# Optimization experiments

Hardware: AMD Instinct MI355X
Metric: run time of the kernel (lower is better)

The kernel has to match this reference:

```python
import jax, jax.numpy as jnp
import numpy as np

N_NODES = 50000
N_EDGES = 400000
IN_FEAT = 988
HIDDEN = 256
CLASSES = 47


def _sage_layer(h, src, dst, W_self, W_neigh, b):
    # DGL SAGEConv 'mean': mean over in-neighbors (messages flow src->dst)
    n = h.shape[0]
    deg = jax.ops.segment_sum(jnp.ones(dst.shape, h.dtype), dst, num_segments=n)
    deg = jnp.maximum(deg, 1.0)  # zero-in-degree nodes -> zero neighbor feature
    agg = jax.ops.segment_sum(h[src], dst, num_segments=n) / deg[:, None]
    return h @ W_self + agg @ W_neigh + b


def setup_inputs() -> dict:
    key = jax.random.key(0)
    ks = jax.random.split(key, 16)
    x = jax.random.normal(ks[0], (N_NODES, IN_FEAT), dtype=jnp.float32)
    src = jax.random.randint(ks[1], (N_EDGES,), 0, N_NODES, dtype=jnp.int32)
    dst = jax.random.randint(ks[2], (N_EDGES,), 0, N_NODES, dtype=jnp.int32)
    dims = [(IN_FEAT, HIDDEN), (HIDDEN, HIDDEN), (HIDDEN, CLASSES)]
    inp = {"x": x, "src": src, "dst": dst}
    for l, (fi, fo) in enumerate(dims):
        s = 1.0 / np.sqrt(fi)
        inp[f"W_self{l}"] = jax.random.normal(ks[3 + 3 * l], (fi, fo), dtype=jnp.float32) * s
        inp[f"W_neigh{l}"] = jax.random.normal(ks[4 + 3 * l], (fi, fo), dtype=jnp.float32) * s
        inp[f"b{l}"] = jnp.zeros((fo,), dtype=jnp.float32)
    return inp


def reference(x, src, dst, W_self0, W_neigh0, b0, W_self1, W_neigh1, b1, W_self2, W_neigh2, b2):
    # feat_size path: h = x, then n_layers SAGEConv layers with relu between
    h = _sage_layer(x, src, dst, W_self0, W_neigh0, b0)
    h = jax.nn.relu(h)
    h = _sage_layer(h, src, dst, W_self1, W_neigh1, b1)
    h = jax.nn.relu(h)
    h = _sage_layer(h, src, dst, W_self2, W_neigh2, b2)
    return h
```

## Files before the change

### kernel.cpp

```cpp
#include <hip/hip_runtime.h>
#include <hip/hip_bf16.h>
#include <cstdint>

#define NODES 50000
#define EDGES 400000
#define FIN   988
#define KP    1024
#define FH    256
#define FC    47

typedef __attribute__((ext_vector_type(8))) short short8;
typedef __attribute__((ext_vector_type(4))) float f32x4;

__device__ __forceinline__ ushort f2bf(float x) {
    union { float f; uint32_t u; } v; v.f = x;
    uint32_t r = v.u + 0x7FFF + ((v.u >> 16) & 1);
    return (ushort)(r >> 16);
}
__device__ __forceinline__ float bf2f(ushort u) {
    union { uint32_t u; float f; } v; v.u = ((uint32_t)u) << 16;
    return v.f;
}
__device__ __forceinline__ void g2l16(const void* g, void* l) {
    __builtin_amdgcn_global_load_lds((const __attribute__((address_space(1))) void*)g,
                                     (__attribute__((address_space(3))) void*)l, 16, 0, 0);
}

__global__ void k_zero(int* __restrict__ p, int n) {
    int i = blockIdx.x * blockDim.x + threadIdx.x;
    if (i < n) p[i] = 0;
}

#define CVTX_BLKS (NODES * (KP / 8) / 256)
#define DEG_BLKS  ((EDGES + 255) / 256)
__global__ void k_cvtx_deg(const float* __restrict__ x, ushort* __restrict__ xbf,
                           const int* __restrict__ dst, int* __restrict__ deg) {
    const int b = blockIdx.x;
    if (b < CVTX_BLKS) {
        int gid = b * 256 + threadIdx.x;
        const int r  = gid >> 7;
        const int kb = (gid & 127) << 3;
        const float* p = x + (size_t)r * FIN + kb;
        short8 o;
        if (kb + 8 <= FIN) {
            f32x4 v0 = *(const f32x4*)(p);
            f32x4 v1 = *(const f32x4*)(p + 4);
#pragma unroll
            for (int i = 0; i < 4; ++i) {
                o[i] = (short)f2bf(v0[i]);
                o[4 + i] = (short)f2bf(v1[i]);
            }
        } else {
#pragma unroll
            for (int i = 0; i < 8; ++i) {
                float f = (kb + i < FIN) ? p[i] : 0.f;
                o[i] = (short)f2bf(f);
            }
        }
        *(short8*)&xbf[(size_t)r * KP + kb] = o;
    } else {
        int i = (b - CVTX_BLKS) * 256 + threadIdx.x;
        if (i < EDGES) atomicAdd(&deg[dst[i]], 1);
    }
}

__global__ __launch_bounds__(256) void k_scan1(const int* __restrict__ deg,
                                               int* __restrict__ bsum, int n) {
    __shared__ int ws[4];
    int i = blockIdx.x * 256 + threadIdx.x;
    int v = (i < n) ? deg[i] : 0;
#pragma unroll
    for (int off = 32; off; off >>= 1) v += __shfl_down(v, off);
    if ((threadIdx.x & 63) == 0) ws[threadIdx.x >> 6] = v;
    __syncthreads();
    if (threadIdx.x == 0) bsum[blockIdx.x] = ws[0] + ws[1] + ws[2] + ws[3];
}

__global__ __launch_bounds__(256) void k_scan2(int* __restrict__ bsum, int nb) {
    __shared__ int s[256];
    int t = threadIdx.x;
    int v = (t < nb) ? bsum[t] : 0;
    s[t] = v;
    __syncthreads();
    for (int off = 1; off < 256; off <<= 1) {
        int u = (t >= off) ? s[t - off] : 0;
        __syncthreads();
        s[t] += u;
        __syncthreads();
    }
    if (t < nb) bsum[t] = s[t] - v;
}

__global__ __launch_bounds__(256) void k_scan3(const int* __restrict__ deg,
                                               const int* __restrict__ bsum,
                                               int* __restrict__ rowptr,
                                               int* __restrict__ cursor, int n) {
    __shared__ int s[256];
    int t = threadIdx.x;
    int i = blockIdx.x * 256 + t;
    int v = (i < n) ? deg[i] : 0;
    s[t] = v;
    __syncthreads();
    for (int off = 1; off < 256; off <<= 1) {
        int u = (t >= off) ? s[t - off] : 0;
        __syncthreads();
        s[t] += u;
        __syncthreads();
    }
    if (i < n) {
        int excl = bsum[blockIdx.x] + s[t] - v;
        rowptr[i] = excl;
        cursor[i] = excl;
    }
    if (i == 0) rowptr[n] = EDGES;
}

#define W0E (512 * KP)
#define W1E (512 * FH)
#define W2E (128 * FH)
#define CVTW_BLKS ((W0E + W1E + W2E + 255) / 256)
__global__ void k_fill_cvtw(const int* __restrict__ src, const int* __restrict__ dst,
                            int* __restrict__ cursor, int* __restrict__ eidx,
                            const float* __restrict__ Ws0, const float* __restrict__ Wn0,
                            const float* __restrict__ Ws1, const float* __restrict__ Wn1,
                            const float* __restrict__ Ws2, const float* __restrict__ Wn2,
                            ushort* __restrict__ Wt0, ushort* __restrict__ Wt1,
                            ushort* __restrict__ Wt2) {
    const int b = blockIdx.x;
    if (b < DEG_BLKS) {
        int i = b * 256 + threadIdx.x;
        if (i < EDGES) {
            int d = dst[i];
            int p = atomicAdd(&cursor[d], 1);
            eidx[p] = src[i];
        }
    } else {
        int gid = (b - DEG_BLKS) * 256 + threadIdx.x;
        if (gid < W0E) {
            int k = gid >> 9, n = gid & 511;
            float v = 0.f;
            if (k < FIN) v = (n < FH) ? Ws0[(size_t)k * FH + n] : Wn0[(size_t)k * FH + (n - FH)];
            Wt0[(size_t)n * KP + k] = f2bf(v);
        } else if (gid < W0E + W1E) {
            int gg = gid - W0E;
            int k = gg >> 9, n = gg & 511;
            float v = (n < FH) ? Ws1[(size_t)k * FH + n] : Wn1[(size_t)k * FH + (n - FH)];
            Wt1[(size_t)n * FH + k] = f2bf(v);
        } else if (gid < W0E + W1E + W2E) {
            int gg = gid - W0E - W1E;
            int k = gg >> 7, n = gg & 127;
            float v = 0.f;
            if (n < FC) v = Ws2[(size_t)k * FC + n];
            else if (n >= 64 && n < 64 + FC) v = Wn2[(size_t)k * FC + (n - 64)];
            Wt2[(size_t)n * FH + k] = f2bf(v);
        }
    }
}

#define TBK 16384

__global__ __launch_bounds__(512, 2) void k_mm256(const ushort* __restrict__ A,
                                                  const ushort* __restrict__ Bt,
                                                  ushort* __restrict__ C,
                                                  const int M, const int lda,
                                                  const int Kpad, const int ldc,
                                                  const int nbx) {
    const int nwg = gridDim.x;
    const int bid = blockIdx.x;
    const int q = nwg >> 3, r = nwg & 7;
    const int xcd = bid & 7, ii = bid >> 3;
    const int swz = (xcd < r ? xcd * (q + 1) : r * (q + 1) + (xcd - r) * q) + ii;
    const int bm = (swz / nbx) * 256;
    const int bn = (swz % nbx) * 256;

    __shared__ ushort As[2 * TBK];
    __shared__ ushort Bs[2 * TBK];

    const int t = threadIdx.x;
    const int wid = t >> 6, lane = t & 63;
    const int wr = (wid >> 2) * 128, wc = (wid & 3) * 64;
    const int lr = lane & 15, g = lane >> 4;

    f32x4 acc[8][4] = {};

    const ushort* asrc[4]; const ushort* bsrc[4]; int cdst[4];
#pragma unroll
    for (int jj = 0; jj < 4; ++jj) {
        const int c = jj * 8 + wid;
        const int row = c * 8 + (lane >> 3);
        const int soff = ((lane & 7) ^ (row & 7)) << 3;
        const int arow = min(bm + row, M - 1);
        asrc[jj] = A + (size_t)arow * lda + soff;
        bsrc[jj] = Bt + (size_t)(bn + row) * Kpad + soff;
        cdst[jj] = c * 512;
    }

    int roA[2][8], roB[2][4];
#pragma unroll
    for (int m = 0; m < 8; ++m) {
        const int rr = wr + m * 16 + lr;
#pragma unroll
        for (int h = 0; h < 2; ++h)
            roA[h][m] = rr * 64 + ((((h << 2) + g) ^ (rr & 7)) << 3);
    }
#pragma unroll
    for (int n = 0; n < 4; ++n) {
        const int col = wc + n * 16 + lr;
#pragma unroll
        for (int h = 0; h < 2; ++h)
            roB[h][n] = col * 64 + ((((h << 2) + g) ^ (col & 7)) << 3);
    }

    auto stage = [&](int tile) {
        const int k0 = tile * 64;
        const int ho = (tile & 1) * TBK;
#pragma unroll
        for (int jj = 0; jj < 4; ++jj) g2l16(asrc[jj] + k0, &As[ho + cdst[jj]]);
#pragma unroll
        for (int jj = 0; jj < 4; ++jj) g2l16(bsrc[jj] + k0, &Bs[ho + cdst[jj]]);
    };

    const int nt = Kpad / 64;
    stage(0);
    if (nt > 1) stage(1);

    for (int it = 0; it < nt; ++it) {
        if (it + 1 < nt) asm volatile("s_waitcnt vmcnt(8)" ::: "memory");
        else             asm volatile("s_waitcnt vmcnt(0)" ::: "memory");
        __builtin_amdgcn_s_barrier();
        __builtin_amdgcn_sched_barrier(0);

        const ushort* Ab = &As[(it & 1) * TBK];
        const ushort* Bb = &Bs[(it & 1) * TBK];
        short8 a0[8], b0[4], a1[8], b1[4];
#pragma unroll
        for (int m = 0; m < 8; ++m) a0[m] = *(const short8*)&Ab[roA[0][m]];
#pragma unroll
        for (int n = 0; n < 4; ++n) b0[n] = *(const short8*)&Bb[roB[0][n]];
#pragma unroll
        for (int m = 0; m < 8; ++m) a1[m] = *(const short8*)&Ab[roA[1][m]];
#pragma unroll
        for (int n = 0; n < 4; ++n) b1[n] = *(const short8*)&Bb[roB[1][n]];

        __builtin_amdgcn_s_setprio(1);
#pragma unroll
        for (int m = 0; m < 8; ++m)
#pragma unroll
            for (int n = 0; n < 4; ++n)
                acc[m][n] = __builtin_amdgcn_mfma_f32_16x16x32_bf16(a0[m], b0[n], acc[m][n], 0, 0, 0);
        __builtin_amdgcn_s_setprio(0);

        asm volatile("s_waitcnt lgkmcnt(0)" ::: "memory");
        __builtin_amdgcn_sched_barrier(0);
        __builtin_amdgcn_s_barrier();
        __builtin_amdgcn_sched_barrier(0);

        if (it + 2 < nt) stage(it + 2);

        __builtin_amdgcn_s_setprio(1);
#pragma unroll
        for (int m = 0; m < 8; ++m)
#pragma unroll
            for (int n = 0; n < 4; ++n)
                acc[m][n] = __builtin_amdgcn_mfma_f32_16x16x32_bf16(a1[m], b1[n], acc[m][n], 0, 0, 0);
        __builtin_amdgcn_s_setprio(0);
    }

#pragma unroll
    for (int m = 0; m < 8; ++m) {
#pragma unroll
        for (int i = 0; i < 4; ++i) {
            const int row = bm + wr + m * 16 + g * 4 + i;
            if (row >= M) continue;
#pragma unroll
            for (int n = 0; n < 4; ++n) {
                const int col = bn + wc + n * 16 + lr;
                C[(size_t)row * ldc + col] = f2bf(acc[m][n][i]);
            }
        }
    }
}

#define BMT 128
#define TBUF 4096
#define NBUF 5

__global__ __launch_bounds__(256, 4) void k_mm(const ushort* __restrict__ A,
                                               const ushort* __restrict__ Bt,
                                               ushort* __restrict__ C,
                                               const int M, const int lda,
                                               const int Kpad, const int ldc,
                                               const int nbx) {
    const int nwg = gridDim.x;
    const int bid = blockIdx.x;
    const int q = nwg >> 3, r = nwg & 7;
    const int xcd = bid & 7, ii = bid >> 3;
    const int swz = (xcd < r ? xcd * (q + 1) : r * (q + 1) + (xcd - r) * q) + ii;
    const int bm = (swz / nbx) * BMT;
    const int bn = (swz % nbx) * BMT;

    __shared__ ushort As[NBUF * TBUF];
    __shared__ ushort Bs[NBUF * TBUF];

    const int t = threadIdx.x;
    const int wid = t >> 6, lane = t & 63;
    const int wr = (wid >> 1) * 64, wc = (wid & 1) * 64;
    const int lr = lane & 15, g = lane >> 4;

    f32x4 acc[4][4] = {};

    const ushort* asrc[2]; const ushort* bsrc[2]; int cdst[2];
#pragma unroll
    for (int j = 0; j < 2; ++j) {
        const int c = j * 4 + wid;
        const int row = c * 16 + (lane >> 2);
        const int soff = (((lane & 3) ^ ((row >> 1) & 3)) << 3);
        const int arow = min(bm + row, M - 1);
        asrc[j] = A + (size_t)arow * lda + soff;
        bsrc[j] = Bt + (size_t)(bn + row) * Kpad + soff;
        cdst[j] = c * 512;
    }

    int roA[4], roB[4];
#pragma unroll
    for (int m = 0; m < 4; ++m) {
        const int row = wr + m * 16 + lr;
        roA[m] = row * 32 + ((g ^ ((row >> 1) & 3)) << 3);
    }
#pragma unroll
    for (int n = 0; n < 4; ++n) {
        const int col = wc + n * 16 + lr;
        roB[n] = col * 32 + ((g ^ ((col >> 1) & 3)) << 3);
    }

    auto stage = [&](int tile) {
        const int k0 = tile * 32;
        const int ho = (tile % NBUF) * TBUF;
        g2l16(asrc[0] + k0, &As[ho + cdst[0]]);
        g2l16(asrc[1] + k0, &As[ho + cdst[1]]);
        g2l16(bsrc[0] + k0, &Bs[ho + cdst[0]]);
        g2l16(bsrc[1] + k0, &Bs[ho + cdst[1]]);
    };

    const int nt = Kpad / 32;
#pragma unroll
    for (int p = 0; p < 4; ++p) if (p < nt) stage(p);

    for (int it = 0; it < nt; ++it) {
        const int rmn = nt - 1 - it;
        if (rmn >= 3)      asm volatile("s_waitcnt vmcnt(12)" ::: "memory");
        else if (rmn == 2) asm volatile("s_waitcnt vmcnt(8)"  ::: "memory");
        else if (rmn == 1) asm volatile("s_waitcnt vmcnt(4)"  ::: "memory");
        else               asm volatile("s_waitcnt vmcnt(0)"  ::: "memory");
        __builtin_amdgcn_s_barrier();
        __builtin_amdgcn_sched_barrier(0);

        if (it + 4 < nt) stage(it + 4);

        const ushort* Ab = &As[(it % NBUF) * TBUF];
        const ushort* Bb = &Bs[(it % NBUF) * TBUF];
        short8 af[4], bfr[4];
#pragma unroll
        for (int m = 0; m < 4; ++m) af[m] = *(const short8*)&Ab[roA[m]];
#pragma unroll
        for (int n = 0; n < 4; ++n) bfr[n] = *(const short8*)&Bb[roB[n]];
        __builtin_amdgcn_s_setprio(1);
#pragma unroll
        for (int m = 0; m < 4; ++m)
#pragma unroll
            for (int n = 0; n < 4; ++n)
                acc[m][n] = __builtin_amdgcn_mfma_f32_16x16x32_bf16(af[m], bfr[n], acc[m][n], 0, 0, 0);
        __builtin_amdgcn_s_setprio(0);
    }

#pragma unroll
    for (int m = 0; m < 4; ++m) {
#pragma unroll
        for (int i = 0; i < 4; ++i) {
            const int row = bm + wr + m * 16 + g * 4 + i;
            if (row >= M) continue;
#pragma unroll
            for (int n = 0; n < 4; ++n) {
                const int col = bn + wc + n * 16 + lr;
                C[(size_t)row * ldc + col] = f2bf(acc[m][n][i]);
            }
        }
    }
}

__global__ void k_gac256(const ushort* __restrict__ C, const int* __restrict__ rowptr,
                         const int* __restrict__ eidx, const float* __restrict__ bias,
                         ushort* __restrict__ hout) {
    int gid = blockIdx.x * blockDim.x + threadIdx.x;
    int node = gid >> 6;
    if (node >= NODES) return;
    const int lane = gid & 63;
    const int l4 = lane << 2;
    const int beg = rowptr[node];
    const int end = rowptr[node + 1];
    const int cnt = end - beg;
    const int pre = min(cnt, 64);
    int myeid = (lane < pre) ? eidx[beg + lane] : 0;

    float a0 = 0.f, a1 = 0.f, a2 = 0.f, a3 = 0.f;
    int i = 0;
    for (; i + 7 < pre; i += 8) {
        int s0 = __shfl(myeid, i),     s1 = __shfl(myeid, i + 1);
        int s2 = __shfl(myeid, i + 2), s3 = __shfl(myeid, i + 3);
        int s4 = __shfl(myeid, i + 4), s5 = __shfl(myeid, i + 5);
        int s6 = __shfl(myeid, i + 6), s7 = __shfl(myeid, i + 7);
        const ushort4 v0 = *(const ushort4*)&C[(size_t)s0 * 512 + 256 + l4];
        const ushort4 v1 = *(const ushort4*)&C[(size_t)s1 * 512 + 256 + l4];
        const ushort4 v2 = *(const ushort4*)&C[(size_t)s2 * 512 + 256 + l4];
        const ushort4 v3 = *(const ushort4*)&C[(size_t)s3 * 512 + 256 + l4];
        const ushort4 v4 = *(const ushort4*)&C[(size_t)s4 * 512 + 256 + l4];
        const ushort4 v5 = *(const ushort4*)&C[(size_t)s5 * 512 + 256 + l4];
        const ushort4 v6 = *(const ushort4*)&C[(size_t)s6 * 512 + 256 + l4];
        const ushort4 v7 = *(const ushort4*)&C[(size_t)s7 * 512 + 256 + l4];
        a0 += ((bf2f(v0.x) + bf2f(v1.x)) + (bf2f(v2.x) + bf2f(v3.x)))
            + ((bf2f(v4.x) + bf2f(v5.x)) + (bf2f(v6.x) + bf2f(v7.x)));
        a1 += ((bf2f(v0.y) + bf2f(v1.y)) + (bf2f(v2.y) + bf2f(v3.y)))
            + ((bf2f(v4.y) + bf2f(v5.y)) + (bf2f(v6.y) + bf2f(v7.y)));
        a2 += ((bf2f(v0.z) + bf2f(v1.z)) + (bf2f(v2.z) + bf2f(v3.z)))
            + ((bf2f(v4.z) + bf2f(v5.z)) + (bf2f(v6.z) + bf2f(v7.z)));
        a3 += ((bf2f(v0.w) + bf2f(v1.w)) + (bf2f(v2.w) + bf2f(v3.w)))
            + ((bf2f(v4.w) + bf2f(v5.w)) + (bf2f(v6.w) + bf2f(v7.w)));
    }
    for (; i < pre; ++i) {
        int s = __shfl(myeid, i);
        const ushort4 v = *(const ushort4*)&C[(size_t)s * 512 + 256 + l4];
        a0 += bf2f(v.x); a1 += bf2f(v.y); a2 += bf2f(v.z); a3 += bf2f(v.w);
    }
    for (int e = beg + 64; e < end; ++e) {
        int s = eidx[e];
        const ushort4 v = *(const ushort4*)&C[(size_t)s * 512 + 256 + l4];
        a0 += bf2f(v.x); a1 += bf2f(v.y); a2 += bf2f(v.z); a3 += bf2f(v.w);
    }
    const float inv = 1.f / (float)max(cnt, 1);
    const ushort4 hs = *(const ushort4*)&C[(size_t)node * 512 + l4];
    const f32x4 bv = *(const f32x4*)&bias[l4];
    ushort4 w;
    w.x = f2bf(fmaxf(bf2f(hs.x) + a0 * inv + bv[0], 0.f));
    w.y = f2bf(fmaxf(bf2f(hs.y) + a1 * inv + bv[1], 0.f));
    w.z = f2bf(fmaxf(bf2f(hs.z) + a2 * inv + bv[2], 0.f));
    w.w = f2bf(fmaxf(bf2f(hs.w) + a3 * inv + bv[3], 0.f));
    *(ushort4*)&hout[(size_t)node * 256 + l4] = w;
}

__global__ void k_gac47(const ushort* __restrict__ C, const int* __restrict__ rowptr,
                        const int* __restrict__ eidx, const float* __restrict__ bias,
                        float* __restrict__ out) {
    int gid = blockIdx.x * blockDim.x + threadIdx.x;
    int wv = gid >> 6;
    const int lane = gid & 63;
    const int sub = lane >> 5, l = lane & 31;
    int node = wv * 2 + sub;
    if (node >= NODES) return;
    const uint32_t* C32 = (const uint32_t*)C;
    const int beg = rowptr[node];
    const int end = rowptr[node + 1];
    const int cnt = end - beg;
    const int pre = min(cnt, 32);
    int myeid = (l < pre) ? eidx[beg + l] : 0;

    float a0 = 0.f, a1 = 0.f;
    if (l < 24) {
        int i = 0;
        for (; i + 3 < pre; i += 4) {
            int s0 = __shfl(myeid, i,     32);
            int s1 = __shfl(myeid, i + 1, 32);
            int s2 = __shfl(myeid, i + 2, 32);
            int s3 = __shfl(myeid, i + 3, 32);
            const uint32_t u0 = C32[(size_t)s0 * 64 + 32 + l];
            const uint32_t u1 = C32[(size_t)s1 * 64 + 32 + l];
            const uint32_t u2 = C32[(size_t)s2 * 64 + 32 + l];
            const uint32_t u3 = C32[(size_t)s3 * 64 + 32 + l];
            a0 += (bf2f((ushort)u0) + bf2f((ushort)u1)) + (bf2f((ushort)u2) + bf2f((ushort)u3));
            a1 += (bf2f((ushort)(u0 >> 16)) + bf2f((ushort)(u1 >> 16)))
                + (bf2f((ushort)(u2 >> 16)) + bf2f((ushort)(u3 >> 16)));
        }
        for (; i < pre; ++i) {
            int s = __shfl(myeid, i, 32);
            const uint32_t u = C32[(size_t)s * 64 + 32 + l];
            a0 += bf2f((ushort)u);
            a1 += bf2f((ushort)(u >> 16));
        }
        for (int e = beg + 32; e < end; ++e) {
            const uint32_t u = C32[(size_t)eidx[e] * 64 + 32 + l];
            a0 += bf2f((ushort)u);
            a1 += bf2f((ushort)(u >> 16));
        }
        const float inv = 1.f / (float)max(cnt, 1);
        const uint32_t us = C32[(size_t)node * 64 + l];
        const int c0 = 2 * l, c1 = 2 * l + 1;
        out[(size_t)node * FC + c0] = bf2f((ushort)us) + a0 * inv + bias[c0];
        if (c1 < FC)
            out[(size_t)node * FC + c1] = bf2f((ushort)(us >> 16)) + a1 * inv + bias[c1];
    }
}

extern "C" void kernel_launch(void* const* d_in, const int* in_sizes, int n_in,
                              void* d_out, int out_size, void* d_ws, size_t ws_size,
                              hipStream_t stream) {
    const float* x       = (const float*)d_in[0];
    const int*   src     = (const int*)d_in[1];
    const int*   dst     = (const int*)d_in[2];
    const float* Wself0  = (const float*)d_in[3];
    const float* Wneigh0 = (const float*)d_in[4];
    const float* b0      = (const float*)d_in[5];
    const float* Wself1  = (const float*)d_in[6];
    const float* Wneigh1 = (const float*)d_in[7];
    const float* b1      = (const float*)d_in[8];
    const float* Wself2  = (const float*)d_in[9];
    const float* Wneigh2 = (const float*)d_in[10];
    const float* b2      = (const float*)d_in[11];
    float* out = (float*)d_out;

    char* w = (char*)d_ws;
    ushort* Cbuf = (ushort*)w;   w += (size_t)NODES * 512 * 2;
    ushort* xbf  = (ushort*)w;   w += (size_t)NODES * KP * 2;
    ushort* hbuf = xbf;
    ushort* Wt0  = (ushort*)w;   w += (size_t)W0E * 2;
    ushort* Wt1  = (ushort*)w;   w += (size_t)W1E * 2;
    ushort* Wt2  = (ushort*)w;   w += (size_t)W2E * 2;
    int* rowptr  = (int*)w;      w += (NODES + 1) * sizeof(int);
    int* cursor  = (int*)w;      w += NODES * sizeof(int);
    int* degarr  = (int*)w;      w += NODES * sizeof(int);
    int* bsum    = (int*)w;      w += 256 * sizeof(int);
    int* eidx    = (int*)w;

    dim3 blk(256);
    const int nblk = (NODES + 255) / 256;

    k_zero<<<nblk, blk, 0, stream>>>(degarr, NODES);
    k_cvtx_deg<<<CVTX_BLKS + DEG_BLKS, blk, 0, stream>>>(x, xbf, dst, degarr);
    k_scan1<<<nblk, blk, 0, stream>>>(degarr, bsum, NODES);
    k_scan2<<<1, blk, 0, stream>>>(bsum, nblk);
    k_scan3<<<nblk, blk, 0, stream>>>(degarr, bsum, rowptr, cursor, NODES);
    k_fill_cvtw<<<DEG_BLKS + CVTW_BLKS, blk, 0, stream>>>(
        src, dst, cursor, eidx,
        Wself0, Wneigh0, Wself1, Wneigh1, Wself2, Wneigh2, Wt0, Wt1, Wt2);

    const int gat_blocks   = (int)(((size_t)NODES * 64 + 255) / 256);
    const int gat47_blocks = (int)((((size_t)NODES + 1) / 2 * 64 + 255) / 256);
    const int nbyM2 = (NODES + 255) / 256;
    const int nbyM  = (NODES + BMT - 1) / BMT;

    k_mm256<<<dim3(2 * nbyM2), dim3(512), 0, stream>>>(xbf, Wt0, Cbuf, NODES, KP, KP, 512, 2);
    k_gac256<<<gat_blocks, blk, 0, stream>>>(Cbuf, rowptr, eidx, b0, hbuf);

    k_mm256<<<dim3(2 * nbyM2), dim3(512), 0, stream>>>(hbuf, Wt1, Cbuf, NODES, FH, FH, 512, 2);
    k_gac256<<<gat_blocks, blk, 0, stream>>>(Cbuf, rowptr, eidx, b1, hbuf);

    k_mm<<<dim3(nbyM), blk, 0, stream>>>(hbuf, Wt2, Cbuf, NODES, FH, FH, 128, 1);
    k_gac47<<<gat47_blocks, blk, 0, stream>>>(Cbuf, rowptr, eidx, b2, out);
}
```

Measured before the change: 299.4 us.

## Fuse CSR fill and weight conversion into scan and first GEMM prologue

Removes the separate fill/convert kernel. The layer-0 weight conversion now runs in extra blocks of the scan1 kernel. The edge-index CSR fill and the layer-1/2 weight conversion run in the prologue of the first GEMM, under a template flag, while its first tiles are in flight. The gather loops in the 256-wide and 47-class aggregation kernels are rewritten as fixed 8-wide unrolled blocks with masked accumulation. This saves launches and gaps between kernels, but the GEMM prologue now waits on all outstanding loads, adds atomics before the main loop, and the masked gather issues extra loads.

```diff
diff --git a/kernel.cpp b/kernel.cpp
--- a/kernel.cpp
+++ b/kernel.cpp
@@ -64,16 +64,36 @@
     }
 }
 
-__global__ __launch_bounds__(256) void k_scan1(const int* __restrict__ deg,
-                                               int* __restrict__ bsum, int n) {
-    __shared__ int ws[4];
-    int i = blockIdx.x * 256 + threadIdx.x;
-    int v = (i < n) ? deg[i] : 0;
-#pragma unroll
-    for (int off = 32; off; off >>= 1) v += __shfl_down(v, off);
-    if ((threadIdx.x & 63) == 0) ws[threadIdx.x >> 6] = v;
-    __syncthreads();
-    if (threadIdx.x == 0) bsum[blockIdx.x] = ws[0] + ws[1] + ws[2] + ws[3];
+#define W0E (512 * KP)
+#define W1E (512 * FH)
+#define W2E (128 * FH)
+#define CVTW0_BLKS ((W0E + 255) / 256)
+#define SCAN_BLKS  ((NODES + 255) / 256)
+
+__global__ __launch_bounds__(256) void k_scan1_cvtw0(const int* __restrict__ deg,
+                                                     int* __restrict__ bsum, int n,
+                                                     const float* __restrict__ Ws0,
+                                                     const float* __restrict__ Wn0,
+                                                     ushort* __restrict__ Wt0) {
+    const int b = blockIdx.x;
+    if (b < SCAN_BLKS) {
+        __shared__ int ws[4];
+        int i = b * 256 + threadIdx.x;
+        int v = (i < n) ? deg[i] : 0;
+#pragma unroll
+        for (int off = 32; off; off >>= 1) v += __shfl_down(v, off);
+        if ((threadIdx.x & 63) == 0) ws[threadIdx.x >> 6] = v;
+        __syncthreads();
+        if (threadIdx.x == 0) bsum[b] = ws[0] + ws[1] + ws[2] + ws[3];
+    } else {
+        int gid = (b - SCAN_BLKS) * 256 + threadIdx.x;
+        if (gid < W0E) {
+            int k = gid >> 9, n2 = gid & 511;
+            float v = 0.f;
+            if (k < FIN) v = (n2 < FH) ? Ws0[(size_t)k * FH + n2] : Wn0[(size_t)k * FH + (n2 - FH)];
+            Wt0[(size_t)n2 * KP + k] = f2bf(v);
+        }
+    }
 }
 
 __global__ __launch_bounds__(256) void k_scan2(int* __restrict__ bsum, int nb) {
@@ -115,56 +135,25 @@
     if (i == 0) rowptr[n] = EDGES;
 }
 
-#define W0E (512 * KP)
-#define W1E (512 * FH)
-#define W2E (128 * FH)
-#define CVTW_BLKS ((W0E + W1E + W2E + 255) / 256)
-__global__ void k_fill_cvtw(const int* __restrict__ src, const int* __restrict__ dst,
-                            int* __restrict__ cursor, int* __restrict__ eidx,
-                            const float* __restrict__ Ws0, const float* __restrict__ Wn0,
-                            const float* __restrict__ Ws1, const float* __restrict__ Wn1,
-                            const float* __restrict__ Ws2, const float* __restrict__ Wn2,
-                            ushort* __restrict__ Wt0, ushort* __restrict__ Wt1,
-                            ushort* __restrict__ Wt2) {
-    const int b = blockIdx.x;
-    if (b < DEG_BLKS) {
-        int i = b * 256 + threadIdx.x;
-        if (i < EDGES) {
-            int d = dst[i];
-            int p = atomicAdd(&cursor[d], 1);
-            eidx[p] = src[i];
-        }
-    } else {
-        int gid = (b - DEG_BLKS) * 256 + threadIdx.x;
-        if (gid < W0E) {
-            int k = gid >> 9, n = gid & 511;
-            float v = 0.f;
-            if (k < FIN) v = (n < FH) ? Ws0[(size_t)k * FH + n] : Wn0[(size_t)k * FH + (n - FH)];
-            Wt0[(size_t)n * KP + k] = f2bf(v);
-        } else if (gid < W0E + W1E) {
-            int gg = gid - W0E;
-            int k = gg >> 9, n = gg & 511;
-            float v = (n < FH) ? Ws1[(size_t)k * FH + n] : Wn1[(size_t)k * FH + (n - FH)];
-            Wt1[(size_t)n * FH + k] = f2bf(v);
-        } else if (gid < W0E + W1E + W2E) {
-            int gg = gid - W0E - W1E;
-            int k = gg >> 7, n = gg & 127;
-            float v = 0.f;
-            if (n < FC) v = Ws2[(size_t)k * FC + n];
-            else if (n >= 64 && n < 64 + FC) v = Wn2[(size_t)k * FC + (n - 64)];
-            Wt2[(size_t)n * FH + k] = f2bf(v);
-        }
-    }
-}
-
 #define TBK 16384
 
+template<int AUX>
 __global__ __launch_bounds__(512, 2) void k_mm256(const ushort* __restrict__ A,
                                                   const ushort* __restrict__ Bt,
                                                   ushort* __restrict__ C,
                                                   const int M, const int lda,
                                                   const int Kpad, const int ldc,
-                                                  const int nbx) {
+                                                  const int nbx,
+                                                  const int* __restrict__ srcp,
+                                                  const int* __restrict__ dstp,
+                                                  int* __restrict__ cursor,
+                                                  int* __restrict__ eidx,
+                                                  const float* __restrict__ Ws1,
+                                                  const float* __restrict__ Wn1,
+                                                  const float* __restrict__ Ws2,
+                                                  const float* __restrict__ Wn2,
+                                                  ushort* __restrict__ Wt1o,
+                                                  ushort* __restrict__ Wt2o) {
     const int nwg = gridDim.x;
     const int bid = blockIdx.x;
     const int q = nwg >> 3, r = nwg & 7;
@@ -223,6 +212,31 @@
     const int nt = Kpad / 64;
     stage(0);
     if (nt > 1) stage(1);
+
+    if constexpr (AUX) {
+        const int rawtid = bid * 512 + t;
+        if (rawtid * 2 + 1 < EDGES) {
+            int2 d2 = ((const int2*)dstp)[rawtid];
+            int2 s2 = ((const int2*)srcp)[rawtid];
+            int p0 = atomicAdd(&cursor[d2.x], 1); eidx[p0] = s2.x;
+            int p1 = atomicAdd(&cursor[d2.y], 1); eidx[p1] = s2.y;
+        }
+        if (rawtid < W1E + W2E) {
+            if (rawtid < W1E) {
+                int k = rawtid >> 9, n2 = rawtid & 511;
+                float v = (n2 < FH) ? Ws1[(size_t)k * FH + n2] : Wn1[(size_t)k * FH + (n2 - FH)];
+                Wt1o[(size_t)n2 * FH + k] = f2bf(v);
+            } else {
+                int gg = rawtid - W1E;
+                int k = gg >> 7, n2 = gg & 127;
+                float v = 0.f;
+                if (n2 < FC) v = Ws2[(size_t)k * FC + n2];
+                else if (n2 >= 64 && n2 < 64 + FC) v = Wn2[(size_t)k * FC + (n2 - 64)];
+                Wt2o[(size_t)n2 * FH + k] = f2bf(v);
+            }
+        }
+        asm volatile("s_waitcnt vmcnt(0)" ::: "memory");
+    }
 
     for (int it = 0; it < nt; ++it) {
         if (it + 1 < nt) asm volatile("s_waitcnt vmcnt(8)" ::: "memory");
@@ -403,33 +417,18 @@
     int myeid = (lane < pre) ? eidx[beg + lane] : 0;
 
     float a0 = 0.f, a1 = 0.f, a2 = 0.f, a3 = 0.f;
-    int i = 0;
-    for (; i + 7 < pre; i += 8) {
-        int s0 = __shfl(myeid, i),     s1 = __shfl(myeid, i + 1);
-        int s2 = __shfl(myeid, i + 2), s3 = __shfl(myeid, i + 3);
-        int s4 = __shfl(myeid, i + 4), s5 = __shfl(myeid, i + 5);
-        int s6 = __shfl(myeid, i + 6), s7 = __shfl(myeid, i + 7);
-        const ushort4 v0 = *(const ushort4*)&C[(size_t)s0 * 512 + 256 + l4];
-        const ushort4 v1 = *(const ushort4*)&C[(size_t)s1 * 512 + 256 + l4];
-        const ushort4 v2 = *(const ushort4*)&C[(size_t)s2 * 512 + 256 + l4];
-        const ushort4 v3 = *(const ushort4*)&C[(size_t)s3 * 512 + 256 + l4];
-        const ushort4 v4 = *(const ushort4*)&C[(size_t)s4 * 512 + 256 + l4];
-        const ushort4 v5 = *(const ushort4*)&C[(size_t)s5 * 512 + 256 + l4];
-        const ushort4 v6 = *(const ushort4*)&C[(size_t)s6 * 512 + 256 + l4];
-        const ushort4 v7 = *(const ushort4*)&C[(size_t)s7 * 512 + 256 + l4];
-        a0 += ((bf2f(v0.x) + bf2f(v1.x)) + (bf2f(v2.x) + bf2f(v3.x)))
-            + ((bf2f(v4.x) + bf2f(v5.x)) + (bf2f(v6.x) + bf2f(v7.x)));
-        a1 += ((bf2f(v0.y) + bf2f(v1.y)) + (bf2f(v2.y) + bf2f(v3.y)))
-            + ((bf2f(v4.y) + bf2f(v5.y)) + (bf2f(v6.y) + bf2f(v7.y)));
-        a2 += ((bf2f(v0.z) + bf2f(v1.z)) + (bf2f(v2.z) + bf2f(v3.z)))
-            + ((bf2f(v4.z) + bf2f(v5.z)) + (bf2f(v6.z) + bf2f(v7.z)));
-        a3 += ((bf2f(v0.w) + bf2f(v1.w)) + (bf2f(v2.w) + bf2f(v3.w)))
-            + ((bf2f(v4.w) + bf2f(v5.w)) + (bf2f(v6.w) + bf2f(v7.w)));
-    }
-    for (; i < pre; ++i) {
-        int s = __shfl(myeid, i);
-        const ushort4 v = *(const ushort4*)&C[(size_t)s * 512 + 256 + l4];
-        a0 += bf2f(v.x); a1 += bf2f(v.y); a2 += bf2f(v.z); a3 += bf2f(v.w);
+    for (int i = 0; i < pre; i += 8) {
+#pragma unroll
+        for (int j = 0; j < 8; ++j) {
+            const int ij = i + j;
+            const bool ok = ij < pre;
+            const int s = __shfl(myeid, ok ? ij : 0);
+            const ushort4 v = *(const ushort4*)&C[(size_t)s * 512 + 256 + l4];
+            if (ok) {
+                a0 += bf2f(v.x); a1 += bf2f(v.y);
+                a2 += bf2f(v.z); a3 += bf2f(v.w);
+            }
+        }
     }
     for (int e = beg + 64; e < end; ++e) {
         int s = eidx[e];
@@ -465,25 +464,18 @@
 
     float a0 = 0.f, a1 = 0.f;
     if (l < 24) {
-        int i = 0;
-        for (; i + 3 < pre; i += 4) {
-            int s0 = __shfl(myeid, i,     32);
-            int s1 = __shfl(myeid, i + 1, 32);
-            int s2 = __shfl(myeid, i + 2, 32);
-            int s3 = __shfl(myeid, i + 3, 32);
-            const uint32_t u0 = C32[(size_t)s0 * 64 + 32 + l];
-            const uint32_t u1 = C32[(size_t)s1 * 64 + 32 + l];
-            const uint32_t u2 = C32[(size_t)s2 * 64 + 32 + l];
-            const uint32_t u3 = C32[(size_t)s3 * 64 + 32 + l];
-            a0 += (bf2f((ushort)u0) + bf2f((ushort)u1)) + (bf2f((ushort)u2) + bf2f((ushort)u3));
-            a1 += (bf2f((ushort)(u0 >> 16)) + bf2f((ushort)(u1 >> 16)))
-                + (bf2f((ushort)(u2 >> 16)) + bf2f((ushort)(u3 >> 16)));
-        }
-        for (; i < pre; ++i) {
-            int s = __shfl(myeid, i, 32);
-            const uint32_t u = C32[(size_t)s * 64 + 32 + l];
-            a0 += bf2f((ushort)u);
-            a1 += bf2f((ushort)(u >> 16));
+        for (int i = 0; i < pre; i += 8) {
+#pragma unroll
+            for (int j = 0; j < 8; ++j) {
+                const int ij = i + j;
+                const bool ok = ij < pre;
+                const int s = __shfl(myeid, ok ? ij : 0, 32);
+                const uint32_t u = C32[(size_t)s * 64 + 32 + l];
+                if (ok) {
+                    a0 += bf2f((ushort)u);
+                    a1 += bf2f((ushort)(u >> 16));
+                }
+            }
         }
         for (int e = beg + 32; e < end; ++e) {
             const uint32_t u = C32[(size_t)eidx[e] * 64 + 32 + l];
@@ -530,26 +522,28 @@
     int* eidx    = (int*)w;
 
     dim3 blk(256);
-    const int nblk = (NODES + 255) / 256;
-
-    k_zero<<<nblk, blk, 0, stream>>>(degarr, NODES);
+
+    k_zero<<<SCAN_BLKS, blk, 0, stream>>>(degarr, NODES);
     k_cvtx_deg<<<CVTX_BLKS + DEG_BLKS, blk, 0, stream>>>(x, xbf, dst, degarr);
-    k_scan1<<<nblk, blk, 0, stream>>>(degarr, bsum, NODES);
-    k_scan2<<<1, blk, 0, stream>>>(bsum, nblk);
-    k_scan3<<<nblk, blk, 0, stream>>>(degarr, bsum, rowptr, cursor, NODES);
-    k_fill_cvtw<<<DEG_BLKS + CVTW_BLKS, blk, 0, stream>>>(
-        src, dst, cursor, eidx,
-        Wself0, Wneigh0, Wself1, Wneigh1, Wself2, Wneigh2, Wt0, Wt1, Wt2);
+    k_scan1_cvtw0<<<SCAN_BLKS + CVTW0_BLKS, blk, 0, stream>>>(
+        degarr, bsum, NODES, Wself0, Wneigh0, Wt0);
+    k_scan2<<<1, blk, 0, stream>>>(bsum, SCAN_BLKS);
+    k_scan3<<<SCAN_BLKS, blk, 0, stream>>>(degarr, bsum, rowptr, cursor, NODES);
 
     const int gat_blocks   = (int)(((size_t)NODES * 64 + 255) / 256);
     const int gat47_blocks = (int)((((size_t)NODES + 1) / 2 * 64 + 255) / 256);
     const int nbyM2 = (NODES + 255) / 256;
     const int nbyM  = (NODES + BMT - 1) / BMT;
 
-    k_mm256<<<dim3(2 * nbyM2), dim3(512), 0, stream>>>(xbf, Wt0, Cbuf, NODES, KP, KP, 512, 2);
+    k_mm256<1><<<dim3(2 * nbyM2), dim3(512), 0, stream>>>(
+        xbf, Wt0, Cbuf, NODES, KP, KP, 512, 2,
+        src, dst, cursor, eidx, Wself1, Wneigh1, Wself2, Wneigh2, Wt1, Wt2);
     k_gac256<<<gat_blocks, blk, 0, stream>>>(Cbuf, rowptr, eidx, b0, hbuf);
 
-    k_mm256<<<dim3(2 * nbyM2), dim3(512), 0, stream>>>(hbuf, Wt1, Cbuf, NODES, FH, FH, 512, 2);
+    k_mm256<0><<<dim3(2 * nbyM2), dim3(512), 0, stream>>>(
+        hbuf, Wt1, Cbuf, NODES, FH, FH, 512, 2,
+        nullptr, nullptr, nullptr, nullptr, nullptr, nullptr, nullptr, nullptr,
+        nullptr, nullptr);
     k_gac256<<<gat_blocks, blk, 0, stream>>>(Cbuf, rowptr, eidx, b1, hbuf);
 
     k_mm<<<dim3(nbyM), blk, 0, stream>>>(hbuf, Wt2, Cbuf, NODES, FH, FH, 128, 1);
```

New measurement: 306.9 us. +2.5%, slower.
